# Kernel optimization log

Measured on AMD Instinct MI355X. Metric: run time of the kernel, lower is better.

The kernel has to match this reference:

```python
import jax, jax.numpy as jnp
import numpy as np

TOP_K = 2
HEAD_NUM = 16


def setup_inputs() -> dict:
    key = jax.random.key(0)
    ks = jax.random.split(key, 6)
    B, H, N, D, G = 8, HEAD_NUM, 2048, 64, 128
    return {
        "q": jax.random.normal(ks[0], (B, H, N, D), dtype=jnp.float32),
        "k": jax.random.normal(ks[1], (B, H, N, D), dtype=jnp.float32),
        "v": jax.random.normal(ks[2], (B, H, N, D), dtype=jnp.float32),
        "gating_input": jax.random.normal(ks[3], (B, N, G), dtype=jnp.float32),
        "rank3_ninf_mask": jnp.zeros((B, N, N), dtype=jnp.float32),
        "W_gate": jax.random.normal(ks[4], (H, G), dtype=jnp.float32) * 0.02,
        "b_gate": jnp.zeros((H,), dtype=jnp.float32),
    }


def reference(q, k, v, gating_input, rank3_ninf_mask, W_gate, b_gate):
    B = q.shape[0]
    d = q.shape[-1]
    # --- router ---
    gate_logits = gating_input.mean(axis=1) @ W_gate.T + b_gate      # [B, H]
    gate_softmax = jax.nn.softmax(gate_logits, axis=1)               # [B, H]
    _, top_k_idx = jax.lax.top_k(gate_softmax, TOP_K)                # [B, K]
    gating_mask = jnp.zeros_like(gate_softmax).at[
        jnp.arange(B)[:, None], top_k_idx].set(1.0)
    # load balancing loss
    tokens_per_expert = gating_mask.sum(axis=0)                      # [H]
    density = tokens_per_expert / (tokens_per_expert.sum() + 1e-6)
    lb_loss = HEAD_NUM * jnp.sum(gate_softmax.mean(axis=0) * density)
    # --- gather selected heads: [B, K, N, D] ---
    idx = top_k_idx[:, :, None, None]
    q_sel = jnp.take_along_axis(q, idx, axis=1)
    k_sel = jnp.take_along_axis(k, idx, axis=1)
    v_sel = jnp.take_along_axis(v, idx, axis=1)
    # --- scaled dot attention ---
    score = jnp.einsum('bhqd,bhkd->bhqk', q_sel, k_sel) / jnp.sqrt(
        jnp.asarray(d, dtype=q.dtype))                               # [B,K,N,N]
    score = score + rank3_ninf_mask[:, None, :, :]
    weights = jax.nn.softmax(score, axis=3)
    out = jnp.einsum('bhqk,bhkd->bhqd', weights, v_sel)              # [B,K,N,D]
    B_, K_, N_, D_ = out.shape
    out = out.transpose(0, 2, 1, 3).reshape(B_, N_, K_ * D_)         # [B,N,K*D]
    return out, lb_loss
```

## Files before the change

### kernel.cpp

```cpp
#include <hip/hip_runtime.h>

#define NSEQ 2048
#define DH 64
#define NH 16
#define BKV 64
#define BQ 128
#define PSTRIDE 8448

typedef __attribute__((ext_vector_type(8))) short bf16x8;
typedef __attribute__((ext_vector_type(4))) short s16x4;
typedef __attribute__((ext_vector_type(16))) float f32x16;
typedef __attribute__((ext_vector_type(4))) unsigned u32x4;

static __device__ __forceinline__ short f2bf(float f) {
    __bf16 b = (__bf16)f;
    return __builtin_bit_cast(short, b);
}

__global__ void gate_partial(const float* __restrict__ gi, float* __restrict__ wsA, int SL) {
    int b = blockIdx.x / SL, sl = blockIdx.x % SL;
    int rows = NSEQ / SL;
    int tid = threadIdx.x;
    int g = tid & 127, half = tid >> 7;
    float s = 0.f;
    int n0 = sl * rows;
    for (int n = n0 + half; n < n0 + rows; n += 2)
        s += gi[((size_t)b * NSEQ + n) * 128 + g];
    __shared__ float part[2][128];
    part[half][g] = s;
    __syncthreads();
    if (tid < 128) wsA[(b * SL + sl) * 128 + tid] = part[0][tid] + part[1][tid];
}

__global__ void gate_final(const float* __restrict__ wsA, const float* __restrict__ Wg,
                           const float* __restrict__ bg, float* __restrict__ ws_sm,
                           int* __restrict__ ws_idx, int SL) {
    int b = blockIdx.x, tid = threadIdx.x;
    __shared__ float meanv[128];
    __shared__ float logits[NH];
    if (tid < 128) {
        float s = 0.f;
        for (int sl = 0; sl < SL; ++sl) s += wsA[(b * SL + sl) * 128 + tid];
        meanv[tid] = s * (1.0f / NSEQ);
    }
    __syncthreads();
    if (tid < 128) {
        int h = tid >> 3, j = tid & 7;
        float p = 0.f;
        for (int i = 0; i < 16; ++i) { int g = j + 8 * i; p += meanv[g] * Wg[h * 128 + g]; }
        p += __shfl_xor(p, 1);
        p += __shfl_xor(p, 2);
        p += __shfl_xor(p, 4);
        if (j == 0) logits[h] = p + bg[h];
    }
    __syncthreads();
    if (tid == 0) {
        float mx = logits[0];
        for (int h = 1; h < NH; ++h) mx = fmaxf(mx, logits[h]);
        float e[NH], sum = 0.f;
        for (int h = 0; h < NH; ++h) { e[h] = __expf(logits[h] - mx); sum += e[h]; }
        float inv = 1.0f / sum;
        for (int h = 0; h < NH; ++h) ws_sm[b * NH + h] = e[h] * inv;
        int i1 = 0;
        for (int h = 1; h < NH; ++h) if (logits[h] > logits[i1]) i1 = h;
        int i2 = (i1 == 0) ? 1 : 0;
        for (int h = 0; h < NH; ++h) if (h != i1 && logits[h] > logits[i2]) i2 = h;
        ws_idx[b * 2 + 0] = i1;
        ws_idx[b * 2 + 1] = i2;
    }
}

static __device__ __forceinline__ void lb_compute(const float* ws_sm, const int* ws_idx,
                                                  float* out_lb) {
    float counts[NH];
    for (int h = 0; h < NH; ++h) counts[h] = 0.f;
    for (int i = 0; i < 16; ++i) counts[ws_idx[i]] += 1.0f;
    float lb = 0.f;
    for (int h = 0; h < NH; ++h) {
        float msm = 0.f;
        for (int b = 0; b < 8; ++b) msm += ws_sm[b * NH + h];
        msm *= (1.0f / 8.0f);
        lb += msm * (counts[h] / (16.0f + 1e-6f));
    }
    out_lb[0] = lb * (float)NH;
}

__global__ void lb_kernel(const float* __restrict__ ws_sm, const int* __restrict__ ws_idx,
                          float* __restrict__ out_lb) {
    if (threadIdx.x == 0 && blockIdx.x == 0) lb_compute(ws_sm, ws_idx, out_lb);
}

template<int SPLIT>
__global__ __launch_bounds__(256, 3)
void attn_kernel(const float* __restrict__ q, const float* __restrict__ k,
                 const float* __restrict__ v, const float* __restrict__ mask,
                 const int* __restrict__ topk, float* __restrict__ out,
                 float* __restrict__ part) {
    const int qt = blockIdx.x & 15;
    const int sp = blockIdx.x >> 4;
    const int kk = blockIdx.y;
    const int b  = blockIdx.z;
    const int hh = topk[b * 2 + kk];
    const int tid = threadIdx.x;
    const int wave = tid >> 6;
    const int lane = tid & 63;
    const int lq = lane & 31;
    const int hi = lane >> 5;

    const int nt = 32 / SPLIT;
    const int t_begin = sp * nt;

    __shared__ short Kb[2][64][72];
    __shared__ short Vt[2][64][72];
    __shared__ float scb[4][32];

    const float QSC = 0.125f * 1.4426950408889634f;
    const float MSC = 1.4426950408889634f;
    const float THR = 10.0f;

    const size_t headoff = ((size_t)b * NH + hh) * (size_t)NSEQ * DH;
    const int qbase = qt * BQ + wave * 32;

    bf16x8 qf[4];
    {
        const float* qp = q + headoff + (size_t)(qbase + lq) * DH;
        #pragma unroll
        for (int dk = 0; dk < 4; ++dk) {
            const float* p = qp + dk * 16 + hi * 8;
            float4 a = *(const float4*)p;
            float4 c = *(const float4*)(p + 4);
            bf16x8 f = { f2bf(a.x * QSC), f2bf(a.y * QSC), f2bf(a.z * QSC), f2bf(a.w * QSC),
                         f2bf(c.x * QSC), f2bf(c.y * QSC), f2bf(c.z * QSC), f2bf(c.w * QSC) };
            qf[dk] = f;
        }
    }

    f32x16 acc0, acc1;
    #pragma unroll
    for (int r = 0; r < 16; ++r) { acc0[r] = 0.f; acc1[r] = 0.f; }
    float m_r = -1e30f, l_r = 0.f;

    const float* kb = k + headoff;
    const float* vb = v + headoff;
    const float* mb = mask + (size_t)b * NSEQ * NSEQ + (size_t)(qbase + lq) * NSEQ;

    const int krow = tid >> 3;
    const int kcol = (tid & 7) * 8;
    const int vrow = (tid & 15) * 4;
    const int vcol = (tid >> 4) * 4;

    float4 kreg[4], vreg[4], mreg[8];

    auto issue_kv = [&](int t0) {
        const float* kp = kb + (size_t)(t0 + krow) * DH + kcol;
        kreg[0] = *(const float4*)kp;
        kreg[1] = *(const float4*)(kp + 4);
        kreg[2] = *(const float4*)(kp + 32 * DH);
        kreg[3] = *(const float4*)(kp + 32 * DH + 4);
        const float* vp = vb + (size_t)(t0 + vrow) * DH + vcol;
        #pragma unroll
        for (int i = 0; i < 4; ++i) vreg[i] = *(const float4*)(vp + i * DH);
    };
    auto issue_mask = [&](int t0) {
        const float* mp = mb + t0 + hi * 4;
        #pragma unroll
        for (int g = 0; g < 4; ++g) {
            mreg[g]     = *(const float4*)(mp + g * 8);
            mreg[4 + g] = *(const float4*)(mp + 32 + g * 8);
        }
    };
    auto stage = [&](int par) {
        bf16x8 k0 = { f2bf(kreg[0].x), f2bf(kreg[0].y), f2bf(kreg[0].z), f2bf(kreg[0].w),
                      f2bf(kreg[1].x), f2bf(kreg[1].y), f2bf(kreg[1].z), f2bf(kreg[1].w) };
        bf16x8 k1 = { f2bf(kreg[2].x), f2bf(kreg[2].y), f2bf(kreg[2].z), f2bf(kreg[2].w),
                      f2bf(kreg[3].x), f2bf(kreg[3].y), f2bf(kreg[3].z), f2bf(kreg[3].w) };
        *(bf16x8*)&Kb[par][krow][kcol] = k0;
        *(bf16x8*)&Kb[par][krow + 32][kcol] = k1;
        s16x4 c0v = { f2bf(vreg[0].x), f2bf(vreg[1].x), f2bf(vreg[2].x), f2bf(vreg[3].x) };
        s16x4 c1v = { f2bf(vreg[0].y), f2bf(vreg[1].y), f2bf(vreg[2].y), f2bf(vreg[3].y) };
        s16x4 c2v = { f2bf(vreg[0].z), f2bf(vreg[1].z), f2bf(vreg[2].z), f2bf(vreg[3].z) };
        s16x4 c3v = { f2bf(vreg[0].w), f2bf(vreg[1].w), f2bf(vreg[2].w), f2bf(vreg[3].w) };
        *(s16x4*)&Vt[par][vcol + 0][vrow] = c0v;
        *(s16x4*)&Vt[par][vcol + 1][vrow] = c1v;
        *(s16x4*)&Vt[par][vcol + 2][vrow] = c2v;
        *(s16x4*)&Vt[par][vcol + 3][vrow] = c3v;
    };

    auto pack2 = [&](float a, float bb) -> unsigned {
        union { short s[2]; unsigned u; } t;
        t.s[0] = f2bf(a); t.s[1] = f2bf(bb);
        return t.u;
    };
    auto buildfrag = [&](float a0, float a1, float a2, float a3,
                         float a4, float a5, float a6, float a7) -> bf16x8 {
        unsigned pk01 = pack2(a0, a1), pk23 = pack2(a2, a3);
        unsigned pk45 = pack2(a4, a5), pk67 = pack2(a6, a7);
        unsigned ta = hi ? pk01 : pk45;
        unsigned tb = hi ? pk23 : pk67;
        unsigned ya = __shfl_xor(ta, 32);
        unsigned yb = __shfl_xor(tb, 32);
        u32x4 fr = { hi ? ya : pk01, hi ? yb : pk23,
                     hi ? pk45 : ya, hi ? pk67 : yb };
        return __builtin_bit_cast(bf16x8, fr);
    };

    issue_kv(t_begin * BKV);
    issue_mask(t_begin * BKV);
    stage(0);
    if (nt > 1) issue_kv((t_begin + 1) * BKV);

    for (int t = 0; t < nt; ++t) {
        const int t0 = (t_begin + t) * BKV;
        const int cur = t & 1;
        __syncthreads();

        f32x16 S0, S1;
        #pragma unroll
        for (int r = 0; r < 16; ++r) { S0[r] = 0.f; S1[r] = 0.f; }
        #pragma unroll
        for (int dk = 0; dk < 4; ++dk) {
            bf16x8 kf0 = *(const bf16x8*)&Kb[cur][lq][dk * 16 + hi * 8];
            bf16x8 kf1 = *(const bf16x8*)&Kb[cur][32 + lq][dk * 16 + hi * 8];
            S0 = __builtin_amdgcn_mfma_f32_32x32x16_bf16(kf0, qf[dk], S0, 0, 0, 0);
            S1 = __builtin_amdgcn_mfma_f32_32x32x16_bf16(kf1, qf[dk], S1, 0, 0, 0);
        }
        #pragma unroll
        for (int g = 0; g < 4; ++g) {
            S0[4*g+0] = fmaf(mreg[g].x, MSC, S0[4*g+0]);
            S0[4*g+1] = fmaf(mreg[g].y, MSC, S0[4*g+1]);
            S0[4*g+2] = fmaf(mreg[g].z, MSC, S0[4*g+2]);
            S0[4*g+3] = fmaf(mreg[g].w, MSC, S0[4*g+3]);
            S1[4*g+0] = fmaf(mreg[4+g].x, MSC, S1[4*g+0]);
            S1[4*g+1] = fmaf(mreg[4+g].y, MSC, S1[4*g+1]);
            S1[4*g+2] = fmaf(mreg[4+g].z, MSC, S1[4*g+2]);
            S1[4*g+3] = fmaf(mreg[4+g].w, MSC, S1[4*g+3]);
        }
        if (t + 1 < nt) issue_mask(t0 + BKV);

        if (t + 1 < nt) {
            stage(cur ^ 1);
            if (t + 2 < nt) issue_kv(t0 + 2 * BKV);
        }

        float tmx[16];
        #pragma unroll
        for (int r = 0; r < 16; ++r) tmx[r] = fmaxf(S0[r], S1[r]);
        #pragma unroll
        for (int w2 = 8; w2 > 0; w2 >>= 1)
            #pragma unroll
            for (int r = 0; r < 8; ++r) if (r < w2) tmx[r] = fmaxf(tmx[r], tmx[r + w2]);
        float pm = fmaxf(tmx[0], __shfl_xor(tmx[0], 32));

        if (__any(pm > m_r + THR)) {
            float mnew = fmaxf(m_r, pm);
            float scw = __builtin_amdgcn_exp2f(m_r - mnew);
            if (lane < 32) scb[wave][lane] = scw;
            #pragma unroll
            for (int g = 0; g < 4; ++g) {
                float4 s4 = *(const float4*)&scb[wave][hi * 4 + g * 8];
                acc0[4*g+0] *= s4.x; acc1[4*g+0] *= s4.x;
                acc0[4*g+1] *= s4.y; acc1[4*g+1] *= s4.y;
                acc0[4*g+2] *= s4.z; acc1[4*g+2] *= s4.z;
                acc0[4*g+3] *= s4.w; acc1[4*g+3] *= s4.w;
            }
            l_r *= scw; m_r = mnew;
        }
        float ps = 0.f;
        #pragma unroll
        for (int r = 0; r < 16; ++r) { float p = __builtin_amdgcn_exp2f(S0[r] - m_r); ps += p; S0[r] = p; }
        #pragma unroll
        for (int r = 0; r < 16; ++r) { float p = __builtin_amdgcn_exp2f(S1[r] - m_r); ps += p; S1[r] = p; }
        ps += __shfl_xor(ps, 32);
        l_r += ps;

        bf16x8 pf0 = buildfrag(S0[0], S0[1], S0[2],  S0[3],  S0[4],  S0[5],  S0[6],  S0[7]);
        bf16x8 pf1 = buildfrag(S0[8], S0[9], S0[10], S0[11], S0[12], S0[13], S0[14], S0[15]);
        bf16x8 pf2 = buildfrag(S1[0], S1[1], S1[2],  S1[3],  S1[4],  S1[5],  S1[6],  S1[7]);
        bf16x8 pf3 = buildfrag(S1[8], S1[9], S1[10], S1[11], S1[12], S1[13], S1[14], S1[15]);

        #pragma unroll
        for (int c = 0; c < 4; ++c) {
            bf16x8 pf = (c == 0) ? pf0 : (c == 1) ? pf1 : (c == 2) ? pf2 : pf3;
            bf16x8 vf0 = *(const bf16x8*)&Vt[cur][lq][c * 16 + hi * 8];
            bf16x8 vf1 = *(const bf16x8*)&Vt[cur][32 + lq][c * 16 + hi * 8];
            acc0 = __builtin_amdgcn_mfma_f32_32x32x16_bf16(pf, vf0, acc0, 0, 0, 0);
            acc1 = __builtin_amdgcn_mfma_f32_32x32x16_bf16(pf, vf1, acc1, 0, 0, 0);
        }
    }

    if (SPLIT == 1) {
        if (lane < 32) scb[wave][lane] = 1.0f / l_r;
        #pragma unroll
        for (int g = 0; g < 4; ++g) {
            float4 s4 = *(const float4*)&scb[wave][hi * 4 + g * 8];
            #pragma unroll
            for (int j = 0; j < 4; ++j) {
                int qrow = qbase + hi * 4 + g * 8 + j;
                float sc = (j == 0) ? s4.x : (j == 1) ? s4.y : (j == 2) ? s4.z : s4.w;
                float* op = out + ((size_t)b * NSEQ + qrow) * 128 + kk * 64;
                op[lq]      = acc0[4*g+j] * sc;
                op[32 + lq] = acc1[4*g+j] * sc;
            }
        }
    } else {
        float* pp = part + (size_t)((((b * 2 + kk) * 16 + qt) * SPLIT) + sp) * PSTRIDE;
        #pragma unroll
        for (int g = 0; g < 4; ++g) {
            #pragma unroll
            for (int j = 0; j < 4; ++j) {
                int qloc = wave * 32 + hi * 4 + g * 8 + j;
                pp[qloc * 64 + lq]      = acc0[4*g+j];
                pp[qloc * 64 + 32 + lq] = acc1[4*g+j];
            }
        }
        if (lane < 32) {
            int wl = wave * 32 + lane;
            pp[8192 + wl] = m_r;
            pp[8320 + wl] = l_r;
        }
    }
}

template<int SPLIT>
__global__ __launch_bounds__(256)
void combine_kernel(const float* __restrict__ part, float* __restrict__ out,
                    const float* __restrict__ ws_sm, const int* __restrict__ ws_idx,
                    float* __restrict__ out_lb) {
    const int qt = blockIdx.x, kk = blockIdx.y, b = blockIdx.z;
    const float* base = part + (size_t)(((b * 2 + kk) * 16 + qt) * SPLIT) * PSTRIDE;
    const int row = threadIdx.x >> 1;
    const int half = threadIdx.x & 1;

    float M = -1e30f;
    #pragma unroll
    for (int s = 0; s < SPLIT; ++s) M = fmaxf(M, base[(size_t)s * PSTRIDE + 8192 + row]);

    float L = 0.f;
    float4 o[8];
    #pragma unroll
    for (int j = 0; j < 8; ++j) o[j] = make_float4(0.f, 0.f, 0.f, 0.f);

    #pragma unroll
    for (int s = 0; s < SPLIT; ++s) {
        const float* pb = base + (size_t)s * PSTRIDE;
        float w = __builtin_amdgcn_exp2f(pb[8192 + row] - M);
        L += w * pb[8320 + row];
        const float4* ap = (const float4*)(pb + row * 64 + half * 32);
        #pragma unroll
        for (int j = 0; j < 8; ++j) {
            float4 a = ap[j];
            o[j].x += w * a.x; o[j].y += w * a.y;
            o[j].z += w * a.z; o[j].w += w * a.w;
        }
    }
    float inv = 1.0f / L;
    float* op = out + ((size_t)b * NSEQ + qt * BQ + row) * 128 + kk * 64 + half * 32;
    #pragma unroll
    for (int j = 0; j < 8; ++j) {
        float4 r = make_float4(o[j].x * inv, o[j].y * inv, o[j].z * inv, o[j].w * inv);
        ((float4*)op)[j] = r;
    }
    if (qt == 0 && kk == 0 && b == 0 && threadIdx.x == 0)
        lb_compute(ws_sm, ws_idx, out_lb);
}

extern "C" void kernel_launch(void* const* d_in, const int* in_sizes, int n_in,
                              void* d_out, int out_size, void* d_ws, size_t ws_size,
                              hipStream_t stream) {
    const float* q    = (const float*)d_in[0];
    const float* k    = (const float*)d_in[1];
    const float* v    = (const float*)d_in[2];
    const float* gi   = (const float*)d_in[3];
    const float* mask = (const float*)d_in[4];
    const float* Wg   = (const float*)d_in[5];
    const float* bg   = (const float*)d_in[6];
    float* out = (float*)d_out;
    float* out_lb = out + (size_t)8 * NSEQ * 128;

    const size_t gateA_bytes = (size_t)8 * 64 * 128 * 4 + 4096;
    const size_t part4 = (size_t)1024 * PSTRIDE * 4;
    const size_t need4 = part4 + gateA_bytes;
    const size_t needB = 65536 + part4;

    int SL, SPLIT;
    float* ws_part;
    float* wsA;
    if (ws_size >= need4) {
        SL = 64; SPLIT = 4;
        ws_part = (float*)d_ws;
        wsA = (float*)((char*)d_ws + part4);
    } else if (ws_size >= needB) {
        SL = 8; SPLIT = 4;
        wsA = (float*)d_ws;
        ws_part = (float*)((char*)d_ws + 65536);
    } else {
        SL = 8; SPLIT = 1;
        wsA = (float*)d_ws;
        ws_part = (float*)d_ws;
    }
    float* ws_sm = wsA + 8 * SL * 128;
    int*   ws_idx = (int*)(ws_sm + 8 * NH);

    gate_partial<<<8 * SL, 256, 0, stream>>>(gi, wsA, SL);
    gate_final<<<8, 256, 0, stream>>>(wsA, Wg, bg, ws_sm, ws_idx, SL);

    if (SPLIT == 4) {
        dim3 grid(16 * 4, 2, 8);
        attn_kernel<4><<<grid, 256, 0, stream>>>(q, k, v, mask, ws_idx, out, ws_part);
        dim3 cgrid(16, 2, 8);
        combine_kernel<4><<<cgrid, 256, 0, stream>>>(ws_part, out, ws_sm, ws_idx, out_lb);
    } else {
        lb_kernel<<<1, 64, 0, stream>>>(ws_sm, ws_idx, out_lb);
        dim3 grid(16, 2, 8);
        attn_kernel<1><<<grid, 256, 0, stream>>>(q, k, v, mask, ws_idx, out, ws_part);
    }
}
```

Baseline: 138.2 us.

## Use 128-wide KV tiles with single LDS buffer and MFMA priority hints

```diff
diff --git a/kernel.cpp b/kernel.cpp
--- a/kernel.cpp
+++ b/kernel.cpp
@@ -3,7 +3,7 @@
 #define NSEQ 2048
 #define DH 64
 #define NH 16
-#define BKV 64
+#define BKV 128
 #define BQ 128
 #define PSTRIDE 8448
 
@@ -107,11 +107,11 @@
     const int lq = lane & 31;
     const int hi = lane >> 5;
 
-    const int nt = 32 / SPLIT;
+    const int nt = NSEQ / (SPLIT * BKV);
     const int t_begin = sp * nt;
 
-    __shared__ short Kb[2][64][72];
-    __shared__ short Vt[2][64][72];
+    __shared__ short Kb[128][72];
+    __shared__ short Vt[64][136];
     __shared__ float scb[4][32];
 
     const float QSC = 0.125f * 1.4426950408889634f;
@@ -144,46 +144,46 @@
     const float* vb = v + headoff;
     const float* mb = mask + (size_t)b * NSEQ * NSEQ + (size_t)(qbase + lq) * NSEQ;
 
-    const int krow = tid >> 3;
-    const int kcol = (tid & 7) * 8;
+    const int krow = tid >> 2;
+    const int kcol = (tid & 3) * 16;
     const int vrow = (tid & 15) * 4;
     const int vcol = (tid >> 4) * 4;
 
-    float4 kreg[4], vreg[4], mreg[8];
-
-    auto issue_kv = [&](int t0) {
-        const float* kp = kb + (size_t)(t0 + krow) * DH + kcol;
-        kreg[0] = *(const float4*)kp;
-        kreg[1] = *(const float4*)(kp + 4);
-        kreg[2] = *(const float4*)(kp + 32 * DH);
-        kreg[3] = *(const float4*)(kp + 32 * DH + 4);
-        const float* vp = vb + (size_t)(t0 + vrow) * DH + vcol;
+    float4 kreg[4], vreg[4], mrgA[8], mrgB[8];
+
+    auto issue_kv = [&](int t0, int half) {
+        const float* kp = kb + (size_t)(t0 + half * 64 + krow) * DH + kcol;
+        #pragma unroll
+        for (int c = 0; c < 4; ++c) kreg[c] = *(const float4*)(kp + c * 4);
+        const float* vp = vb + (size_t)(t0 + half * 64 + vrow) * DH + vcol;
         #pragma unroll
         for (int i = 0; i < 4; ++i) vreg[i] = *(const float4*)(vp + i * DH);
     };
-    auto issue_mask = [&](int t0) {
-        const float* mp = mb + t0 + hi * 4;
-        #pragma unroll
-        for (int g = 0; g < 4; ++g) {
-            mreg[g]     = *(const float4*)(mp + g * 8);
-            mreg[4 + g] = *(const float4*)(mp + 32 + g * 8);
-        }
-    };
-    auto stage = [&](int par) {
+    auto stage_half = [&](int half) {
         bf16x8 k0 = { f2bf(kreg[0].x), f2bf(kreg[0].y), f2bf(kreg[0].z), f2bf(kreg[0].w),
                       f2bf(kreg[1].x), f2bf(kreg[1].y), f2bf(kreg[1].z), f2bf(kreg[1].w) };
         bf16x8 k1 = { f2bf(kreg[2].x), f2bf(kreg[2].y), f2bf(kreg[2].z), f2bf(kreg[2].w),
                       f2bf(kreg[3].x), f2bf(kreg[3].y), f2bf(kreg[3].z), f2bf(kreg[3].w) };
-        *(bf16x8*)&Kb[par][krow][kcol] = k0;
-        *(bf16x8*)&Kb[par][krow + 32][kcol] = k1;
+        *(bf16x8*)&Kb[half * 64 + krow][kcol] = k0;
+        *(bf16x8*)&Kb[half * 64 + krow][kcol + 8] = k1;
         s16x4 c0v = { f2bf(vreg[0].x), f2bf(vreg[1].x), f2bf(vreg[2].x), f2bf(vreg[3].x) };
         s16x4 c1v = { f2bf(vreg[0].y), f2bf(vreg[1].y), f2bf(vreg[2].y), f2bf(vreg[3].y) };
         s16x4 c2v = { f2bf(vreg[0].z), f2bf(vreg[1].z), f2bf(vreg[2].z), f2bf(vreg[3].z) };
         s16x4 c3v = { f2bf(vreg[0].w), f2bf(vreg[1].w), f2bf(vreg[2].w), f2bf(vreg[3].w) };
-        *(s16x4*)&Vt[par][vcol + 0][vrow] = c0v;
-        *(s16x4*)&Vt[par][vcol + 1][vrow] = c1v;
-        *(s16x4*)&Vt[par][vcol + 2][vrow] = c2v;
-        *(s16x4*)&Vt[par][vcol + 3][vrow] = c3v;
+        *(s16x4*)&Vt[vcol + 0][half * 64 + vrow] = c0v;
+        *(s16x4*)&Vt[vcol + 1][half * 64 + vrow] = c1v;
+        *(s16x4*)&Vt[vcol + 2][half * 64 + vrow] = c2v;
+        *(s16x4*)&Vt[vcol + 3][half * 64 + vrow] = c3v;
+    };
+    auto issue_mask = [&](int t0) {
+        const float* mp = mb + t0 + hi * 4;
+        #pragma unroll
+        for (int g = 0; g < 4; ++g) {
+            mrgA[g]     = *(const float4*)(mp + g * 8);
+            mrgA[4 + g] = *(const float4*)(mp + 32 + g * 8);
+            mrgB[g]     = *(const float4*)(mp + 64 + g * 8);
+            mrgB[4 + g] = *(const float4*)(mp + 96 + g * 8);
+        }
     };
 
     auto pack2 = [&](float a, float bb) -> unsigned {
@@ -204,43 +204,31 @@
         return __builtin_bit_cast(bf16x8, fr);
     };
 
-    issue_kv(t_begin * BKV);
-    issue_mask(t_begin * BKV);
-    stage(0);
-    if (nt > 1) issue_kv((t_begin + 1) * BKV);
-
-    for (int t = 0; t < nt; ++t) {
-        const int t0 = (t_begin + t) * BKV;
-        const int cur = t & 1;
-        __syncthreads();
-
+    auto substep = [&](int s, const float4* mrg, bool pf_mask, int next_t0) {
         f32x16 S0, S1;
         #pragma unroll
         for (int r = 0; r < 16; ++r) { S0[r] = 0.f; S1[r] = 0.f; }
+        __builtin_amdgcn_s_setprio(1);
         #pragma unroll
         for (int dk = 0; dk < 4; ++dk) {
-            bf16x8 kf0 = *(const bf16x8*)&Kb[cur][lq][dk * 16 + hi * 8];
-            bf16x8 kf1 = *(const bf16x8*)&Kb[cur][32 + lq][dk * 16 + hi * 8];
+            bf16x8 kf0 = *(const bf16x8*)&Kb[s * 64 + lq][dk * 16 + hi * 8];
+            bf16x8 kf1 = *(const bf16x8*)&Kb[s * 64 + 32 + lq][dk * 16 + hi * 8];
             S0 = __builtin_amdgcn_mfma_f32_32x32x16_bf16(kf0, qf[dk], S0, 0, 0, 0);
             S1 = __builtin_amdgcn_mfma_f32_32x32x16_bf16(kf1, qf[dk], S1, 0, 0, 0);
         }
+        __builtin_amdgcn_s_setprio(0);
         #pragma unroll
         for (int g = 0; g < 4; ++g) {
-            S0[4*g+0] = fmaf(mreg[g].x, MSC, S0[4*g+0]);
-            S0[4*g+1] = fmaf(mreg[g].y, MSC, S0[4*g+1]);
-            S0[4*g+2] = fmaf(mreg[g].z, MSC, S0[4*g+2]);
-            S0[4*g+3] = fmaf(mreg[g].w, MSC, S0[4*g+3]);
-            S1[4*g+0] = fmaf(mreg[4+g].x, MSC, S1[4*g+0]);
-            S1[4*g+1] = fmaf(mreg[4+g].y, MSC, S1[4*g+1]);
-            S1[4*g+2] = fmaf(mreg[4+g].z, MSC, S1[4*g+2]);
-            S1[4*g+3] = fmaf(mreg[4+g].w, MSC, S1[4*g+3]);
-        }
-        if (t + 1 < nt) issue_mask(t0 + BKV);
-
-        if (t + 1 < nt) {
-            stage(cur ^ 1);
-            if (t + 2 < nt) issue_kv(t0 + 2 * BKV);
-        }
+            S0[4*g+0] = fmaf(mrg[g].x, MSC, S0[4*g+0]);
+            S0[4*g+1] = fmaf(mrg[g].y, MSC, S0[4*g+1]);
+            S0[4*g+2] = fmaf(mrg[g].z, MSC, S0[4*g+2]);
+            S0[4*g+3] = fmaf(mrg[g].w, MSC, S0[4*g+3]);
+            S1[4*g+0] = fmaf(mrg[4+g].x, MSC, S1[4*g+0]);
+            S1[4*g+1] = fmaf(mrg[4+g].y, MSC, S1[4*g+1]);
+            S1[4*g+2] = fmaf(mrg[4+g].z, MSC, S1[4*g+2]);
+            S1[4*g+3] = fmaf(mrg[4+g].w, MSC, S1[4*g+3]);
+        }
+        if (pf_mask) issue_mask(next_t0);
 
         float tmx[16];
         #pragma unroll
@@ -278,14 +266,32 @@
         bf16x8 pf2 = buildfrag(S1[0], S1[1], S1[2],  S1[3],  S1[4],  S1[5],  S1[6],  S1[7]);
         bf16x8 pf3 = buildfrag(S1[8], S1[9], S1[10], S1[11], S1[12], S1[13], S1[14], S1[15]);
 
+        __builtin_amdgcn_s_setprio(1);
         #pragma unroll
         for (int c = 0; c < 4; ++c) {
             bf16x8 pf = (c == 0) ? pf0 : (c == 1) ? pf1 : (c == 2) ? pf2 : pf3;
-            bf16x8 vf0 = *(const bf16x8*)&Vt[cur][lq][c * 16 + hi * 8];
-            bf16x8 vf1 = *(const bf16x8*)&Vt[cur][32 + lq][c * 16 + hi * 8];
+            bf16x8 vf0 = *(const bf16x8*)&Vt[lq][s * 64 + c * 16 + hi * 8];
+            bf16x8 vf1 = *(const bf16x8*)&Vt[32 + lq][s * 64 + c * 16 + hi * 8];
             acc0 = __builtin_amdgcn_mfma_f32_32x32x16_bf16(pf, vf0, acc0, 0, 0, 0);
             acc1 = __builtin_amdgcn_mfma_f32_32x32x16_bf16(pf, vf1, acc1, 0, 0, 0);
         }
+        __builtin_amdgcn_s_setprio(0);
+    };
+
+    issue_kv(t_begin * BKV, 0);
+    issue_mask(t_begin * BKV);
+
+    for (int t = 0; t < nt; ++t) {
+        const int t0 = (t_begin + t) * BKV;
+        __syncthreads();
+        stage_half(0);
+        issue_kv(t0, 1);
+        stage_half(1);
+        __syncthreads();
+        if (t + 1 < nt) issue_kv(t0 + BKV, 0);
+
+        substep(0, mrgA, false, 0);
+        substep(1, mrgB, t + 1 < nt, t0 + BKV);
     }
 
     if (SPLIT == 1) {
```

New measurement: 219.4 us. 58.7% more time.
